# Kernel tuning notes

Hardware: AMD Instinct MI355X
Metric: run time of the kernel (lower is better)

## Reference

```python
import jax, jax.numpy as jnp
import numpy as np

N_HEAD = 16
EMBED = 1024
HEAD_DIM = EMBED // N_HEAD  # 64
HALF = HEAD_DIM // 2        # 32
T = 2048                    # total packed tokens
NSEG = 4
SEG = T // NSEG             # 512 tokens per packed sequence
SCALE = HEAD_DIM ** -0.5


def _apply_rotary_vision(t, freqs):
    # t: [T, H, D], freqs: [T, D/2] -> Qwen2-VL style vision RoPE
    cos = jnp.concatenate([jnp.cos(freqs), jnp.cos(freqs)], axis=-1)[:, None, :]  # [T,1,D]
    sin = jnp.concatenate([jnp.sin(freqs), jnp.sin(freqs)], axis=-1)[:, None, :]
    t1, t2 = t[..., :HALF], t[..., HALF:]
    rot = jnp.concatenate([-t2, t1], axis=-1)  # rotate_half
    return t * cos + rot * sin


def setup_inputs() -> dict:
    key = jax.random.key(0)
    k1, k2, k3, k4, k5 = jax.random.split(key, 5)
    hidden_states = jax.random.normal(k1, (T, EMBED), dtype=jnp.float32)
    cu_seqlens = (jnp.arange(NSEG + 1, dtype=jnp.int32) * SEG)  # [0,512,...,2048]
    # realistic rotary freqs: position within each segment * inverse frequencies
    pos = jnp.tile(jnp.arange(SEG, dtype=jnp.float32), NSEG)  # [T]
    inv_freq = 1.0 / (10000.0 ** (jnp.arange(HALF, dtype=jnp.float32) / HALF))
    rotary_pos_emb = pos[:, None] * inv_freq[None, :]  # [T, HALF]
    std = 0.02
    wq = jax.random.normal(k2, (EMBED, EMBED), dtype=jnp.float32) * std
    wk = jax.random.normal(k3, (EMBED, EMBED), dtype=jnp.float32) * std
    wv = jax.random.normal(k4, (EMBED, EMBED), dtype=jnp.float32) * std
    wo = jax.random.normal(k5, (EMBED, EMBED), dtype=jnp.float32) * std
    return {"hidden_states": hidden_states, "cu_seqlens": cu_seqlens,
            "rotary_pos_emb": rotary_pos_emb, "wq": wq, "wk": wk, "wv": wv, "wo": wo}


def reference(hidden_states, cu_seqlens, rotary_pos_emb, wq, wk, wv, wo):
    # QKV projections (nn.Linear, bias=False): y = x @ W.T
    q = (hidden_states @ wq.T).reshape(T, N_HEAD, HEAD_DIM)
    k = (hidden_states @ wk.T).reshape(T, N_HEAD, HEAD_DIM)
    v = (hidden_states @ wv.T).reshape(T, N_HEAD, HEAD_DIM)
    q = _apply_rotary_vision(q, rotary_pos_emb)
    k = _apply_rotary_vision(k, rotary_pos_emb)
    # varlen (block-diagonal, non-causal) attention over packed segments
    seg_id = jnp.searchsorted(cu_seqlens, jnp.arange(T, dtype=cu_seqlens.dtype), side='right')
    same_seg = seg_id[:, None] == seg_id[None, :]  # [T, T]
    scores = jnp.einsum('thd,shd->hts', q, k) * SCALE  # [H, T, T]
    scores = jnp.where(same_seg[None, :, :], scores, jnp.finfo(scores.dtype).min)
    probs = jax.nn.softmax(scores, axis=-1)
    attn = jnp.einsum('hts,shd->thd', probs, v).reshape(T, EMBED)
    return attn @ wo.T
```

## Files before the change

### kernel.cpp

```cpp
#include <hip/hip_runtime.h>
#include <cstdint>

#define T_TOK 2048
#define EMBED 1024
#define NH    16
#define HD    64
#define HALF  32
#define SEG   512
#define SL    (0.125f * 1.44269504088896f)

typedef __attribute__((ext_vector_type(8))) __bf16 bf16x8;
typedef __attribute__((ext_vector_type(4))) float  f32x4;
typedef unsigned short u16;
typedef unsigned int   u32;

__device__ __forceinline__ u16 f2bf(float f) {
  u32 u = __builtin_bit_cast(u32, f);
  u += 0x7fffu + ((u >> 16) & 1u);
  return (u16)(u >> 16);
}

__device__ __forceinline__ void gld_lds16(const void* g, void* l) {
  __builtin_amdgcn_global_load_lds(
      reinterpret_cast<__attribute__((address_space(1))) u32*>(
          reinterpret_cast<uintptr_t>(g)),
      reinterpret_cast<__attribute__((address_space(3))) u32*>(
          reinterpret_cast<uintptr_t>(l)),
      16, 0, 0);
}

__global__ __launch_bounds__(256) void convert_k(
    const float* __restrict__ H,  const float* __restrict__ wq,
    const float* __restrict__ wk, const float* __restrict__ wv,
    const float* __restrict__ wo, u16* __restrict__ dst) {
  const size_t gid = (size_t)blockIdx.x * 256 + threadIdx.x;
  const size_t e = gid * 4;
  const float* src; size_t off;
  const size_t HN = (size_t)T_TOK * EMBED;
  if (e < HN) { src = H; off = e; }
  else {
    size_t r = e - HN;
    int w = (int)(r >> 20);
    off = r & ((1u << 20) - 1);
    src = (w == 0) ? wq : (w == 1) ? wk : (w == 2) ? wv : wo;
  }
  const float4 v = *(const float4*)(src + off);
  ushort4 o;
  o.x = f2bf(v.x); o.y = f2bf(v.y); o.z = f2bf(v.z); o.w = f2bf(v.w);
  *(ushort4*)(dst + e) = o;
}

__global__ __launch_bounds__(256) void qkv_k(
    const u16* __restrict__ Hb, const u16* __restrict__ Wb,
    const float* __restrict__ rope, u16* __restrict__ Qb,
    u16* __restrict__ Kb, u16* __restrict__ Vt) {
  constexpr int K = 1024, N = 1024;
  __shared__ alignas(16) u16 As[2][2][64 * 32];
  __shared__ alignas(16) u16 Bs[2][2][128 * 32];
  const int tid = threadIdx.x;
  const int wave = tid >> 6, lane = tid & 63;
  const int quad = lane >> 4, l16 = lane & 15;
  const int bm = blockIdx.y * 64, bn = blockIdx.x * 128;
  const int z = blockIdx.z;
  const u16* Bz = Wb + ((size_t)z << 20);
  const int wm = (wave >> 1) * 32, wn = (wave & 1) * 64;

  f32x4 acc[2][4];
#pragma unroll
  for (int i = 0; i < 2; ++i)
#pragma unroll
    for (int j = 0; j < 4; ++j) { f32x4 zz = {0.f, 0.f, 0.f, 0.f}; acc[i][j] = zz; }

  const int srow = tid >> 2, scol = (tid & 3) * 8;
  const u16* gA = Hb + (size_t)(bm + srow) * K + scol;
  const u16* gB = Bz + (size_t)(bn + srow) * K + scol;

#pragma unroll
  for (int p = 0; p < 2; ++p) {
    gld_lds16(gA + p * 32, (char*)&As[0][p][0] + wave * 1024);
    gld_lds16(gB + p * 32, (char*)&Bs[0][p][0] + wave * 1024);
    gld_lds16(gB + (size_t)64 * K + p * 32, (char*)&Bs[0][p][64 * 32] + wave * 1024);
  }

  for (int kk = 0; kk < K; kk += 64) {
    __syncthreads();
    const int cur = (kk >> 6) & 1, nxt = cur ^ 1;
    if (kk + 64 < K) {
      const int kn = kk + 64;
#pragma unroll
      for (int p = 0; p < 2; ++p) {
        gld_lds16(gA + kn + p * 32, (char*)&As[nxt][p][0] + wave * 1024);
        gld_lds16(gB + kn + p * 32, (char*)&Bs[nxt][p][0] + wave * 1024);
        gld_lds16(gB + (size_t)64 * K + kn + p * 32,
                  (char*)&Bs[nxt][p][64 * 32] + wave * 1024);
      }
    }
#pragma unroll
    for (int p = 0; p < 2; ++p) {
      const u16* Ac = &As[cur][p][0];
      const u16* Bc = &Bs[cur][p][0];
      bf16x8 af[2], bfv[4];
#pragma unroll
      for (int i = 0; i < 2; ++i)
        af[i] = *(const bf16x8*)(Ac + (wm + i * 16 + l16) * 32 + quad * 8);
#pragma unroll
      for (int j = 0; j < 4; ++j)
        bfv[j] = *(const bf16x8*)(Bc + (wn + j * 16 + l16) * 32 + quad * 8);
#pragma unroll
      for (int i = 0; i < 2; ++i)
#pragma unroll
        for (int j = 0; j < 4; ++j)
          acc[i][j] = __builtin_amdgcn_mfma_f32_16x16x32_bf16(af[i], bfv[j],
                                                              acc[i][j], 0, 0, 0);
    }
  }

  if (z < 2) {
    u16* dst = z ? Kb : Qb;
#pragma unroll
    for (int i = 0; i < 2; ++i)
#pragma unroll
      for (int r = 0; r < 4; ++r) {
        const int t = bm + wm + i * 16 + quad * 4 + r;
        const float f0 = rope[t * HALF + l16];
        const float f1 = rope[t * HALF + 16 + l16];
        float s0, c0, s1, c1;
        __sincosf(f0, &s0, &c0);
        __sincosf(f1, &s1, &c1);
        const float v0 = acc[i][0][r], v1 = acc[i][1][r];
        const float v2 = acc[i][2][r], v3 = acc[i][3][r];
        const size_t base = (size_t)t * N + bn + wn + l16;
        dst[base]      = f2bf(v0 * c0 - v2 * s0);
        dst[base + 16] = f2bf(v1 * c1 - v3 * s1);
        dst[base + 32] = f2bf(v2 * c0 + v0 * s0);
        dst[base + 48] = f2bf(v3 * c1 + v1 * s1);
      }
  } else {
#pragma unroll
    for (int i = 0; i < 2; ++i) {
      const int t0 = bm + wm + i * 16 + quad * 4;
#pragma unroll
      for (int j = 0; j < 4; ++j) {
        const int col = bn + wn + j * 16 + l16;
        ushort4 pk;
        pk.x = f2bf(acc[i][j][0]); pk.y = f2bf(acc[i][j][1]);
        pk.z = f2bf(acc[i][j][2]); pk.w = f2bf(acc[i][j][3]);
        *(ushort4*)(Vt + (size_t)col * T_TOK + t0) = pk;
      }
    }
  }
}

__global__ __launch_bounds__(256) void attn_sk(
    const u16* __restrict__ Qb, const u16* __restrict__ Kb,
    const u16* __restrict__ Vt, u16* __restrict__ Ab) {
  const int b = blockIdx.x;
  const int qtile = b & 127, h = b >> 7;
  const int seg = qtile >> 5;
  const int tid = threadIdx.x;
  const int wave = tid >> 6, lane = tid & 63;
  const int quad = lane >> 4, l16 = lane & 15;

  __shared__ alignas(16) char smem[17920];
  u16*   pw = (u16*)smem + wave * 1152;
  float* Os = (float*)smem;
  float* Mm = (float*)smem + 4 * 16 * 68;
  float* Ll = Mm + 64;

  const int qbase = qtile * 16;
  const u16* qp = Qb + (size_t)(qbase + l16) * EMBED + h * HD + quad * 8;
  const bf16x8 qf0 = *(const bf16x8*)qp;
  const bf16x8 qf1 = *(const bf16x8*)(qp + 32);

  float mold[4] = {-1e30f, -1e30f, -1e30f, -1e30f};
  float lsum[4] = {0.f, 0.f, 0.f, 0.f};
  f32x4 O[4];
#pragma unroll
  for (int nt = 0; nt < 4; ++nt) { f32x4 z = {0.f, 0.f, 0.f, 0.f}; O[nt] = z; }

  for (int cc = 0; cc < 2; ++cc) {
    const int c0 = wave * 128 + cc * 64;
    f32x4 S[4];
#pragma unroll
    for (int kt = 0; kt < 4; ++kt) {
      const u16* kp = Kb + (size_t)(seg * SEG + c0 + kt * 16 + l16) * EMBED +
                      h * HD + quad * 8;
      bf16x8 kf0 = *(const bf16x8*)kp;
      bf16x8 kf1 = *(const bf16x8*)(kp + 32);
      f32x4 s = {0.f, 0.f, 0.f, 0.f};
      s = __builtin_amdgcn_mfma_f32_16x16x32_bf16(qf0, kf0, s, 0, 0, 0);
      s = __builtin_amdgcn_mfma_f32_16x16x32_bf16(qf1, kf1, s, 0, 0, 0);
      S[kt] = s;
    }
    bf16x8 vf0[4], vf1[4];
#pragma unroll
    for (int nt = 0; nt < 4; ++nt) {
      const u16* vp = Vt + (size_t)(h * HD + nt * 16 + l16) * T_TOK +
                      seg * SEG + c0 + quad * 8;
      vf0[nt] = *(const bf16x8*)vp;
      vf1[nt] = *(const bf16x8*)(vp + 32);
    }
    float mx[4], al[4];
#pragma unroll
    for (int r = 0; r < 4; ++r) {
      float m = fmaxf(fmaxf(S[0][r], S[1][r]), fmaxf(S[2][r], S[3][r]));
#pragma unroll
      for (int off = 1; off < 16; off <<= 1) m = fmaxf(m, __shfl_xor(m, off));
      float mn = fmaxf(mold[r], m);
      al[r] = exp2f((mold[r] - mn) * SL);
      mold[r] = mn;
      mx[r] = mn;
    }
    float ps[4] = {0.f, 0.f, 0.f, 0.f};
#pragma unroll
    for (int kt = 0; kt < 4; ++kt)
#pragma unroll
      for (int r = 0; r < 4; ++r) {
        float p = exp2f((S[kt][r] - mx[r]) * SL);
        ps[r] += p;
        pw[(quad * 4 + r) * 72 + kt * 16 + l16] = f2bf(p);
      }
#pragma unroll
    for (int r = 0; r < 4; ++r) lsum[r] = lsum[r] * al[r] + ps[r];
#pragma unroll
    for (int nt = 0; nt < 4; ++nt) {
      O[nt][0] *= al[0]; O[nt][1] *= al[1];
      O[nt][2] *= al[2]; O[nt][3] *= al[3];
    }
    const u16* pp = pw + l16 * 72 + quad * 8;
    bf16x8 pf0 = *(const bf16x8*)pp;
    bf16x8 pf1 = *(const bf16x8*)(pp + 32);
#pragma unroll
    for (int nt = 0; nt < 4; ++nt) {
      O[nt] = __builtin_amdgcn_mfma_f32_16x16x32_bf16(pf0, vf0[nt], O[nt], 0, 0, 0);
      O[nt] = __builtin_amdgcn_mfma_f32_16x16x32_bf16(pf1, vf1[nt], O[nt], 0, 0, 0);
    }
  }
#pragma unroll
  for (int r = 0; r < 4; ++r) {
#pragma unroll
    for (int off = 1; off < 16; off <<= 1) lsum[r] += __shfl_xor(lsum[r], off);
  }

  __syncthreads();
#pragma unroll
  for (int nt = 0; nt < 4; ++nt)
#pragma unroll
    for (int r = 0; r < 4; ++r)
      Os[(wave * 16 + quad * 4 + r) * 68 + nt * 16 + l16] = O[nt][r];
  if (l16 == 0) {
#pragma unroll
    for (int r = 0; r < 4; ++r) {
      Mm[wave * 16 + quad * 4 + r] = mold[r];
      Ll[wave * 16 + quad * 4 + r] = lsum[r];
    }
  }
  __syncthreads();

  const int col = wave * 16 + l16;
#pragma unroll
  for (int r = 0; r < 4; ++r) {
    const int row = quad * 4 + r;
    const float m0 = Mm[row], m1 = Mm[16 + row];
    const float m2 = Mm[32 + row], m3 = Mm[48 + row];
    const float ms = fmaxf(fmaxf(m0, m1), fmaxf(m2, m3));
    const float w0 = exp2f((m0 - ms) * SL), w1 = exp2f((m1 - ms) * SL);
    const float w2 = exp2f((m2 - ms) * SL), w3 = exp2f((m3 - ms) * SL);
    const float ls = w0 * Ll[row] + w1 * Ll[16 + row] +
                     w2 * Ll[32 + row] + w3 * Ll[48 + row];
    const float ov = w0 * Os[row * 68 + col] + w1 * Os[(16 + row) * 68 + col] +
                     w2 * Os[(32 + row) * 68 + col] + w3 * Os[(48 + row) * 68 + col];
    Ab[(size_t)(qbase + row) * EMBED + h * HD + col] = f2bf(ov / ls);
  }
}

__global__ __launch_bounds__(256) void oproj_k(
    const u16* __restrict__ Ab, const u16* __restrict__ Wo,
    float* __restrict__ out) {
  constexpr int K = 1024, N = 1024;
  __shared__ alignas(16) u16 As[2][2][64 * 32];
  __shared__ alignas(16) u16 Bs[2][2][128 * 32];
  const int tid = threadIdx.x;
  const int wave = tid >> 6, lane = tid & 63;
  const int quad = lane >> 4, l16 = lane & 15;
  const int bm = blockIdx.y * 64, bn = blockIdx.x * 128;
  const int wm = (wave >> 1) * 32, wn = (wave & 1) * 64;

  f32x4 acc[2][4];
#pragma unroll
  for (int i = 0; i < 2; ++i)
#pragma unroll
    for (int j = 0; j < 4; ++j) { f32x4 z = {0.f, 0.f, 0.f, 0.f}; acc[i][j] = z; }

  const int srow = tid >> 2, scol = (tid & 3) * 8;
  const u16* gA = Ab + (size_t)(bm + srow) * K + scol;
  const u16* gB = Wo + (size_t)(bn + srow) * K + scol;

#pragma unroll
  for (int p = 0; p < 2; ++p) {
    gld_lds16(gA + p * 32, (char*)&As[0][p][0] + wave * 1024);
    gld_lds16(gB + p * 32, (char*)&Bs[0][p][0] + wave * 1024);
    gld_lds16(gB + (size_t)64 * K + p * 32, (char*)&Bs[0][p][64 * 32] + wave * 1024);
  }

  for (int kk = 0; kk < K; kk += 64) {
    __syncthreads();
    const int cur = (kk >> 6) & 1, nxt = cur ^ 1;
    if (kk + 64 < K) {
      const int kn = kk + 64;
#pragma unroll
      for (int p = 0; p < 2; ++p) {
        gld_lds16(gA + kn + p * 32, (char*)&As[nxt][p][0] + wave * 1024);
        gld_lds16(gB + kn + p * 32, (char*)&Bs[nxt][p][0] + wave * 1024);
        gld_lds16(gB + (size_t)64 * K + kn + p * 32,
                  (char*)&Bs[nxt][p][64 * 32] + wave * 1024);
      }
    }
#pragma unroll
    for (int p = 0; p < 2; ++p) {
      const u16* Ac = &As[cur][p][0];
      const u16* Bc = &Bs[cur][p][0];
      bf16x8 af[2], bfv[4];
#pragma unroll
      for (int i = 0; i < 2; ++i)
        af[i] = *(const bf16x8*)(Ac + (wm + i * 16 + l16) * 32 + quad * 8);
#pragma unroll
      for (int j = 0; j < 4; ++j)
        bfv[j] = *(const bf16x8*)(Bc + (wn + j * 16 + l16) * 32 + quad * 8);
#pragma unroll
      for (int i = 0; i < 2; ++i)
#pragma unroll
        for (int j = 0; j < 4; ++j)
          acc[i][j] = __builtin_amdgcn_mfma_f32_16x16x32_bf16(af[i], bfv[j],
                                                              acc[i][j], 0, 0, 0);
    }
  }

#pragma unroll
  for (int i = 0; i < 2; ++i)
#pragma unroll
    for (int r = 0; r < 4; ++r) {
      const int row = bm + wm + i * 16 + quad * 4 + r;
#pragma unroll
      for (int j = 0; j < 4; ++j)
        out[(size_t)row * N + bn + wn + j * 16 + l16] = acc[i][j][r];
    }
}

extern "C" void kernel_launch(void* const* d_in, const int* in_sizes, int n_in,
                              void* d_out, int out_size, void* d_ws,
                              size_t ws_size, hipStream_t stream) {
  const float* H    = (const float*)d_in[0];
  const float* rope = (const float*)d_in[2];
  const float* wq   = (const float*)d_in[3];
  const float* wk   = (const float*)d_in[4];
  const float* wv   = (const float*)d_in[5];
  const float* wo   = (const float*)d_in[6];
  float* out        = (float*)d_out;

  constexpr size_t M1 = (size_t)1 << 20;
  if (ws_size < 28 * M1) return;

  u16* ws16 = (u16*)d_ws;
  u16* Hb = ws16;
  u16* Wb = ws16 + 2 * M1;
  u16* Qb = ws16 + 6 * M1;
  u16* Kb = ws16 + 8 * M1;
  u16* Vt = ws16 + 10 * M1;
  u16* Ab = ws16 + 12 * M1;

  convert_k<<<6144, 256, 0, stream>>>(H, wq, wk, wv, wo, ws16);
  qkv_k<<<dim3(8, 32, 3), 256, 0, stream>>>(Hb, Wb, rope, Qb, Kb, Vt);
  attn_sk<<<2048, 256, 0, stream>>>(Qb, Kb, Vt, Ab);
  oproj_k<<<dim3(8, 32), 256, 0, stream>>>(Ab, Wb + 3 * M1, out);
}
```

Baseline: 147.5 us.

## Share K/V tiles across waves in LDS and re-layout K/V for contiguous loads

```diff
diff --git a/kernel.cpp b/kernel.cpp
--- a/kernel.cpp
+++ b/kernel.cpp
@@ -53,7 +53,7 @@
 __global__ __launch_bounds__(256) void qkv_k(
     const u16* __restrict__ Hb, const u16* __restrict__ Wb,
     const float* __restrict__ rope, u16* __restrict__ Qb,
-    u16* __restrict__ Kb, u16* __restrict__ Vt) {
+    u16* __restrict__ Khh, u16* __restrict__ Vss) {
   constexpr int K = 1024, N = 1024;
   __shared__ alignas(16) u16 As[2][2][64 * 32];
   __shared__ alignas(16) u16 Bs[2][2][128 * 32];
@@ -115,8 +115,8 @@
     }
   }
 
-  if (z < 2) {
-    u16* dst = z ? Kb : Qb;
+  const int h = (bn + wn) >> 6;
+  if (z == 0) {
 #pragma unroll
     for (int i = 0; i < 2; ++i)
 #pragma unroll
@@ -130,75 +130,113 @@
         const float v0 = acc[i][0][r], v1 = acc[i][1][r];
         const float v2 = acc[i][2][r], v3 = acc[i][3][r];
         const size_t base = (size_t)t * N + bn + wn + l16;
-        dst[base]      = f2bf(v0 * c0 - v2 * s0);
-        dst[base + 16] = f2bf(v1 * c1 - v3 * s1);
-        dst[base + 32] = f2bf(v2 * c0 + v0 * s0);
-        dst[base + 48] = f2bf(v3 * c1 + v1 * s1);
+        Qb[base]      = f2bf(v0 * c0 - v2 * s0);
+        Qb[base + 16] = f2bf(v1 * c1 - v3 * s1);
+        Qb[base + 32] = f2bf(v2 * c0 + v0 * s0);
+        Qb[base + 48] = f2bf(v3 * c1 + v1 * s1);
+      }
+  } else if (z == 1) {
+#pragma unroll
+    for (int i = 0; i < 2; ++i)
+#pragma unroll
+      for (int r = 0; r < 4; ++r) {
+        const int t = bm + wm + i * 16 + quad * 4 + r;
+        const float f0 = rope[t * HALF + l16];
+        const float f1 = rope[t * HALF + 16 + l16];
+        float s0, c0, s1, c1;
+        __sincosf(f0, &s0, &c0);
+        __sincosf(f1, &s1, &c1);
+        const float v0 = acc[i][0][r], v1 = acc[i][1][r];
+        const float v2 = acc[i][2][r], v3 = acc[i][3][r];
+        const size_t b0 = ((size_t)(h * 2 + 0) * T_TOK + t) * 32;
+        const size_t b1 = ((size_t)(h * 2 + 1) * T_TOK + t) * 32;
+        Khh[b0 + l16]      = f2bf(v0 * c0 - v2 * s0);
+        Khh[b0 + 16 + l16] = f2bf(v1 * c1 - v3 * s1);
+        Khh[b1 + l16]      = f2bf(v2 * c0 + v0 * s0);
+        Khh[b1 + 16 + l16] = f2bf(v3 * c1 + v1 * s1);
       }
   } else {
 #pragma unroll
     for (int i = 0; i < 2; ++i) {
       const int t0 = bm + wm + i * 16 + quad * 4;
+      const int tp = t0 >> 5, toff = t0 & 31;
 #pragma unroll
       for (int j = 0; j < 4; ++j) {
-        const int col = bn + wn + j * 16 + l16;
+        const int d = j * 16 + l16;
         ushort4 pk;
         pk.x = f2bf(acc[i][j][0]); pk.y = f2bf(acc[i][j][1]);
         pk.z = f2bf(acc[i][j][2]); pk.w = f2bf(acc[i][j][3]);
-        *(ushort4*)(Vt + (size_t)col * T_TOK + t0) = pk;
-      }
-    }
-  }
-}
-
-__global__ __launch_bounds__(256) void attn_sk(
-    const u16* __restrict__ Qb, const u16* __restrict__ Kb,
-    const u16* __restrict__ Vt, u16* __restrict__ Ab) {
+        *(ushort4*)(Vss + ((size_t)(h * 64 + tp) * 64 + d) * 32 + toff) = pk;
+      }
+    }
+  }
+}
+
+__global__ __launch_bounds__(256) void attn_st(
+    const u16* __restrict__ Qb, const u16* __restrict__ Khh,
+    const u16* __restrict__ Vss, u16* __restrict__ Ab) {
   const int b = blockIdx.x;
-  const int qtile = b & 127, h = b >> 7;
-  const int seg = qtile >> 5;
+  const int qt = b & 7, seg = (b >> 3) & 3, h = b >> 5;
   const int tid = threadIdx.x;
   const int wave = tid >> 6, lane = tid & 63;
   const int quad = lane >> 4, l16 = lane & 15;
 
-  __shared__ alignas(16) char smem[17920];
-  u16*   pw = (u16*)smem + wave * 1152;
-  float* Os = (float*)smem;
-  float* Mm = (float*)smem + 4 * 16 * 68;
-  float* Ll = Mm + 64;
-
-  const int qbase = qtile * 16;
+  __shared__ alignas(16) u16 Ks[2][64 * 32];
+  __shared__ alignas(16) u16 Vs[2][64 * 32];
+  __shared__ alignas(16) u16 Pl[4][16 * 72];
+
+  const int qbase = seg * SEG + qt * 64 + wave * 16;
   const u16* qp = Qb + (size_t)(qbase + l16) * EMBED + h * HD + quad * 8;
   const bf16x8 qf0 = *(const bf16x8*)qp;
   const bf16x8 qf1 = *(const bf16x8*)(qp + 32);
 
+  const u16* Ksrc0 = Khh + ((size_t)(h * 2 + 0) * T_TOK + seg * SEG) * 32;
+  const u16* Ksrc1 = Khh + ((size_t)(h * 2 + 1) * T_TOK + seg * SEG) * 32;
+  const u16* Vsrc  = Vss + ((size_t)(h * 64 + seg * 16) * 64) * 32;
+
   float mold[4] = {-1e30f, -1e30f, -1e30f, -1e30f};
   float lsum[4] = {0.f, 0.f, 0.f, 0.f};
   f32x4 O[4];
 #pragma unroll
   for (int nt = 0; nt < 4; ++nt) { f32x4 z = {0.f, 0.f, 0.f, 0.f}; O[nt] = z; }
 
-  for (int cc = 0; cc < 2; ++cc) {
-    const int c0 = wave * 128 + cc * 64;
+  u16* pw = Pl[wave];
+  const int toff = tid * 8;
+
+  uint4 kreg0 = *(const uint4*)(Ksrc0 + toff);
+  uint4 kreg1 = *(const uint4*)(Ksrc1 + toff);
+  uint4 vreg0 = *(const uint4*)(Vsrc + toff);
+  uint4 vreg1 = *(const uint4*)(Vsrc + 2048 + toff);
+
+  for (int cc = 0; cc < 8; ++cc) {
+    *(uint4*)((char*)&Ks[0][0] + tid * 16) = kreg0;
+    *(uint4*)((char*)&Ks[1][0] + tid * 16) = kreg1;
+    *(uint4*)((char*)&Vs[0][0] + tid * 16) = vreg0;
+    *(uint4*)((char*)&Vs[1][0] + tid * 16) = vreg1;
+    __syncthreads();
+    if (cc + 1 < 8) {
+      const size_t kc = (size_t)(cc + 1) * 2048 + toff;
+      const size_t vc = (size_t)(cc + 1) * 4096 + toff;
+      kreg0 = *(const uint4*)(Ksrc0 + kc);
+      kreg1 = *(const uint4*)(Ksrc1 + kc);
+      vreg0 = *(const uint4*)(Vsrc + vc);
+      vreg1 = *(const uint4*)(Vsrc + vc + 2048);
+    }
     f32x4 S[4];
 #pragma unroll
     for (int kt = 0; kt < 4; ++kt) {
-      const u16* kp = Kb + (size_t)(seg * SEG + c0 + kt * 16 + l16) * EMBED +
-                      h * HD + quad * 8;
-      bf16x8 kf0 = *(const bf16x8*)kp;
-      bf16x8 kf1 = *(const bf16x8*)(kp + 32);
+      const bf16x8 k0 = *(const bf16x8*)&Ks[0][(kt * 16 + l16) * 32 + quad * 8];
+      const bf16x8 k1 = *(const bf16x8*)&Ks[1][(kt * 16 + l16) * 32 + quad * 8];
       f32x4 s = {0.f, 0.f, 0.f, 0.f};
-      s = __builtin_amdgcn_mfma_f32_16x16x32_bf16(qf0, kf0, s, 0, 0, 0);
-      s = __builtin_amdgcn_mfma_f32_16x16x32_bf16(qf1, kf1, s, 0, 0, 0);
+      s = __builtin_amdgcn_mfma_f32_16x16x32_bf16(qf0, k0, s, 0, 0, 0);
+      s = __builtin_amdgcn_mfma_f32_16x16x32_bf16(qf1, k1, s, 0, 0, 0);
       S[kt] = s;
     }
     bf16x8 vf0[4], vf1[4];
 #pragma unroll
     for (int nt = 0; nt < 4; ++nt) {
-      const u16* vp = Vt + (size_t)(h * HD + nt * 16 + l16) * T_TOK +
-                      seg * SEG + c0 + quad * 8;
-      vf0[nt] = *(const bf16x8*)vp;
-      vf1[nt] = *(const bf16x8*)(vp + 32);
+      vf0[nt] = *(const bf16x8*)&Vs[0][(nt * 16 + l16) * 32 + quad * 8];
+      vf1[nt] = *(const bf16x8*)&Vs[1][(nt * 16 + l16) * 32 + quad * 8];
     }
     float mx[4], al[4];
 #pragma unroll
@@ -228,50 +266,29 @@
       O[nt][2] *= al[2]; O[nt][3] *= al[3];
     }
     const u16* pp = pw + l16 * 72 + quad * 8;
-    bf16x8 pf0 = *(const bf16x8*)pp;
-    bf16x8 pf1 = *(const bf16x8*)(pp + 32);
+    const bf16x8 pf0 = *(const bf16x8*)pp;
+    const bf16x8 pf1 = *(const bf16x8*)(pp + 32);
 #pragma unroll
     for (int nt = 0; nt < 4; ++nt) {
       O[nt] = __builtin_amdgcn_mfma_f32_16x16x32_bf16(pf0, vf0[nt], O[nt], 0, 0, 0);
       O[nt] = __builtin_amdgcn_mfma_f32_16x16x32_bf16(pf1, vf1[nt], O[nt], 0, 0, 0);
     }
+    __syncthreads();
   }
 #pragma unroll
   for (int r = 0; r < 4; ++r) {
-#pragma unroll
-    for (int off = 1; off < 16; off <<= 1) lsum[r] += __shfl_xor(lsum[r], off);
-  }
-
-  __syncthreads();
+    float l = lsum[r];
+#pragma unroll
+    for (int off = 1; off < 16; off <<= 1) l += __shfl_xor(l, off);
+    lsum[r] = 1.f / l;
+  }
 #pragma unroll
   for (int nt = 0; nt < 4; ++nt)
 #pragma unroll
-    for (int r = 0; r < 4; ++r)
-      Os[(wave * 16 + quad * 4 + r) * 68 + nt * 16 + l16] = O[nt][r];
-  if (l16 == 0) {
-#pragma unroll
     for (int r = 0; r < 4; ++r) {
-      Mm[wave * 16 + quad * 4 + r] = mold[r];
-      Ll[wave * 16 + quad * 4 + r] = lsum[r];
-    }
-  }
-  __syncthreads();
-
-  const int col = wave * 16 + l16;
-#pragma unroll
-  for (int r = 0; r < 4; ++r) {
-    const int row = quad * 4 + r;
-    const float m0 = Mm[row], m1 = Mm[16 + row];
-    const float m2 = Mm[32 + row], m3 = Mm[48 + row];
-    const float ms = fmaxf(fmaxf(m0, m1), fmaxf(m2, m3));
-    const float w0 = exp2f((m0 - ms) * SL), w1 = exp2f((m1 - ms) * SL);
-    const float w2 = exp2f((m2 - ms) * SL), w3 = exp2f((m3 - ms) * SL);
-    const float ls = w0 * Ll[row] + w1 * Ll[16 + row] +
-                     w2 * Ll[32 + row] + w3 * Ll[48 + row];
-    const float ov = w0 * Os[row * 68 + col] + w1 * Os[(16 + row) * 68 + col] +
-                     w2 * Os[(32 + row) * 68 + col] + w3 * Os[(48 + row) * 68 + col];
-    Ab[(size_t)(qbase + row) * EMBED + h * HD + col] = f2bf(ov / ls);
-  }
+      const int trow = qbase + quad * 4 + r;
+      Ab[(size_t)trow * EMBED + h * HD + nt * 16 + l16] = f2bf(O[nt][r] * lsum[r]);
+    }
 }
 
 __global__ __launch_bounds__(256) void oproj_k(
@@ -362,15 +379,15 @@
   if (ws_size < 28 * M1) return;
 
   u16* ws16 = (u16*)d_ws;
-  u16* Hb = ws16;
-  u16* Wb = ws16 + 2 * M1;
-  u16* Qb = ws16 + 6 * M1;
-  u16* Kb = ws16 + 8 * M1;
-  u16* Vt = ws16 + 10 * M1;
-  u16* Ab = ws16 + 12 * M1;
+  u16* Hb  = ws16;
+  u16* Wb  = ws16 + 2 * M1;
+  u16* Qb  = ws16 + 6 * M1;
+  u16* Khh = ws16 + 8 * M1;
+  u16* Vss = ws16 + 10 * M1;
+  u16* Ab  = ws16 + 12 * M1;
 
   convert_k<<<6144, 256, 0, stream>>>(H, wq, wk, wv, wo, ws16);
-  qkv_k<<<dim3(8, 32, 3), 256, 0, stream>>>(Hb, Wb, rope, Qb, Kb, Vt);
-  attn_sk<<<2048, 256, 0, stream>>>(Qb, Kb, Vt, Ab);
+  qkv_k<<<dim3(8, 32, 3), 256, 0, stream>>>(Hb, Wb, rope, Qb, Khh, Vss);
+  attn_st<<<512, 256, 0, stream>>>(Qb, Khh, Vss, Ab);
   oproj_k<<<dim3(8, 32), 256, 0, stream>>>(Ab, Wb + 3 * M1, out);
 }
```

Result: faster. 132.0 us (-10.5%).
